# Kernel optimization log

Hardware: AMD Instinct MI355X
Metric: run time of the kernel (lower is better)

Reference implementation:

```python
import jax, jax.numpy as jnp
import numpy as np


def setup_inputs() -> dict:
    key = jax.random.key(0)
    k1, k2 = jax.random.split(key)
    f = jax.random.normal(k1, (4, 8192, 3), dtype=jnp.float32)
    f_ = jax.random.normal(k2, (4, 8192, 3), dtype=jnp.float32)
    return {"f": f, "f_": f_}


def _square_distance(src, dst):
    # src: [B,N,3], dst: [B,M,3] -> [B,N,M]
    # ||s-d||^2 = ||s||^2 + ||d||^2 - 2 s.d
    cross = jnp.einsum("bnc,bmc->bnm", src, dst)  # [B,N,M]
    s2 = jnp.sum(src * src, axis=-1)[:, :, None]   # [B,N,1]
    d2 = jnp.sum(dst * dst, axis=-1)[:, None, :]   # [B,1,M]
    return s2 + d2 - 2.0 * cross


def reference(f, f_):
    dis = _square_distance(f, f_)
    dis = jnp.maximum(dis, 0.0)  # dis[dis <= 0] = 0
    f2f_ = jnp.min(dis, axis=2)  # [B,N] nearest in f_ for each point of f
    f_2f = jnp.min(dis, axis=1)  # [B,M] nearest in f for each point of f_
    d = jnp.mean(f2f_, axis=1) + jnp.mean(f_2f, axis=1)  # [B]
    return jnp.mean(d)
```

## Files before the change

kernel.cpp:

```cpp
#include <hip/hip_runtime.h>

#define NPTS  8192
#define BATCH 4

typedef short  bf8    __attribute__((ext_vector_type(8)));
typedef float  f32x16 __attribute__((ext_vector_type(16)));
typedef float  v2f    __attribute__((ext_vector_type(2)));

__device__ inline unsigned short bf16_rne(float x) {
    unsigned u = __float_as_uint(x);
    unsigned r = (u + 0x7FFFu + ((u >> 16) & 1u)) >> 16;
    return (unsigned short)r;
}
__device__ inline float bf16_to_f(unsigned short h) {
    return __uint_as_float(((unsigned)h) << 16);
}
__device__ inline unsigned fenc(float x) {
    unsigned b = __float_as_uint(x);
    return (b & 0x80000000u) ? ~b : (b | 0x80000000u);
}
__device__ inline float fdec(unsigned k) {
    unsigned b = (k & 0x80000000u) ? (k ^ 0x80000000u) : ~k;
    return __uint_as_float(b);
}
template <int CTRL>
__device__ inline float dpp_mov(float x) {
    int i = __float_as_int(x);
    int r = __builtin_amdgcn_update_dpp(i, i, CTRL, 0xF, 0xF, false);
    return __int_as_float(r);
}
__device__ inline float redmax16(f32x16 v) {
    float a = fmaxf(v[0], v[1]),  b = fmaxf(v[2], v[3]);
    float c = fmaxf(v[4], v[5]),  d = fmaxf(v[6], v[7]);
    float e = fmaxf(v[8], v[9]),  f = fmaxf(v[10], v[11]);
    float g = fmaxf(v[12], v[13]), h = fmaxf(v[14], v[15]);
    float ab = fmaxf(a, b), cd = fmaxf(c, d);
    float ef = fmaxf(e, f), gh = fmaxf(g, h);
    return fmaxf(fmaxf(ab, cd), fmaxf(ef, gh));
}


__global__ void pack_mfma(const float* __restrict__ f, const float* __restrict__ f_,
                          bf8* __restrict__ fA, bf8* __restrict__ gB,
                          unsigned* __restrict__ seg, float* __restrict__ out) {
    int j = blockIdx.x * blockDim.x + threadIdx.x;
    if (j == 0) out[0] = 0.0f;
    seg[j] = 0u;
    int cloud = j >> 15;
    int idx   = j & 32767;
    const float* src = cloud ? f_ : f;
    float x = src[idx * 3 + 0], y = src[idx * 3 + 1], z = src[idx * 3 + 2];
    float w = -0.5f * (x * x + y * y + z * z);
    unsigned short xh = bf16_rne(x), yh = bf16_rne(y), zh = bf16_rne(z);
    unsigned short xl = bf16_rne(x - bf16_to_f(xh));
    unsigned short yl = bf16_rne(y - bf16_to_f(yh));
    unsigned short zl = bf16_rne(z - bf16_to_f(zh));
    unsigned short wh = bf16_rne(w);
    unsigned short wl = bf16_rne(w - bf16_to_f(wh));
    const short ONE = (short)0x3F80;

    int b = idx >> 13, p = idx & 8191;
    int t = p >> 5, li = p & 31;
    size_t base = ((size_t)(b * 256 + t)) * 64;
    if (cloud == 0) {
        bf8 A0, A1;
        A0[0]=(short)xh; A0[1]=(short)yh; A0[2]=(short)zh; A0[3]=(short)xl;
        A0[4]=(short)yl; A0[5]=(short)zl; A0[6]=(short)xh; A0[7]=(short)yh;
        A1[0]=(short)zh; A1[1]=ONE;       A1[2]=ONE;       A1[3]=(short)wh;
        A1[4]=(short)wl; A1[5]=0;         A1[6]=0;         A1[7]=0;
        fA[base + li]      = A0;
        fA[base + 32 + li] = A1;
    } else {
        bf8 B0, B1;
        B0[0]=(short)xh; B0[1]=(short)yh; B0[2]=(short)zh; B0[3]=(short)xh;
        B0[4]=(short)yh; B0[5]=(short)zh; B0[6]=(short)xl; B0[7]=(short)yl;
        B1[0]=(short)zl; B1[1]=(short)wh; B1[2]=(short)wl; B1[3]=ONE;
        B1[4]=ONE;       B1[5]=0;         B1[6]=0;         B1[7]=0;
        gB[base + li]      = B0;
        gB[base + 32 + li] = B1;
    }
}

__global__ __launch_bounds__(512, 4) void chamfer_mfma(
        const bf8* __restrict__ fA, const bf8* __restrict__ gB,
        unsigned* __restrict__ seg) {
    __shared__ bf8 lbs[2048];
    __shared__ unsigned colacc[1024];

    int tid  = threadIdx.x;
    int wv   = tid >> 6, lane = tid & 63;
    int bx   = blockIdx.x;
    int mseg = bx & 7;
    int nblk = (bx >> 3) & 15;
    int b    = bx >> 7;

    bf8 a[2];
    f32x16 rmax[2];
    int nt_loc = nblk * 16 + wv * 2;
#pragma unroll
    for (int s = 0; s < 2; ++s) {
        a[s] = fA[(size_t)(b * 256 + nt_loc + s) * 64 + lane];
        rmax[s] = (f32x16)(-3.0e38f);
    }

    const bf8* __restrict__ bp = gB + ((size_t)(b * 256 + mseg * 32)) * 64;
#pragma unroll
    for (int k = 0; k < 4; ++k) lbs[k * 512 + tid] = bp[k * 512 + tid];
    colacc[tid]       = 0u;
    colacc[tid + 512] = 0u;
    __syncthreads();

    f32x16 zc = (f32x16)(0.0f);
    unsigned* cp = &colacc[lane & 31];
    bf8 qa = lbs[lane];
    bf8 qb = lbs[64 + lane];
#pragma unroll 2
    for (int i = 0; i < 16; ++i) {
        int ip = (i + 1) & 15;
        bf8 na = lbs[ip * 128 + lane];
        bf8 nb = lbs[ip * 128 + 64 + lane];
        f32x16 d00 = __builtin_amdgcn_mfma_f32_32x32x16_bf16(a[0], qa, zc, 0, 0, 0);
        f32x16 d01 = __builtin_amdgcn_mfma_f32_32x32x16_bf16(a[0], qb, zc, 0, 0, 0);
        rmax[0] = __builtin_elementwise_max(
                      __builtin_elementwise_max(rmax[0], d00), d01);
        float t00 = redmax16(d00);
        float t01 = redmax16(d01);
        __builtin_amdgcn_sched_barrier(0);
        f32x16 d10 = __builtin_amdgcn_mfma_f32_32x32x16_bf16(a[1], qa, zc, 0, 0, 0);
        f32x16 d11 = __builtin_amdgcn_mfma_f32_32x32x16_bf16(a[1], qb, zc, 0, 0, 0);
        rmax[1] = __builtin_elementwise_max(
                      __builtin_elementwise_max(rmax[1], d10), d11);
        atomicMax(cp + i * 64,      fenc(fmaxf(t00, redmax16(d10))));
        atomicMax(cp + i * 64 + 32, fenc(fmaxf(t01, redmax16(d11))));
        __builtin_amdgcn_sched_barrier(0);
        qa = na; qb = nb;
    }

#pragma unroll
    for (int s = 0; s < 2; ++s) {
#pragma unroll
        for (int r = 0; r < 16; ++r) {
            float x = rmax[s][r];
            x = fmaxf(x, dpp_mov<0xB1>(x));
            x = fmaxf(x, dpp_mov<0x4E>(x));
            x = fmaxf(x, dpp_mov<0x124>(x));
            x = fmaxf(x, dpp_mov<0x128>(x));
            x = fmaxf(x, dpp_mov<0x142>(x));
            rmax[s][r] = x;
        }
    }

    if ((lane & 31) == 16) {
        int rbase = (lane >> 5) * 4;
        unsigned* sg = seg + (size_t)b * NPTS;
#pragma unroll
        for (int s = 0; s < 2; ++s) {
            int n0 = (nt_loc + s) * 32;
#pragma unroll
            for (int r = 0; r < 16; ++r) {
                int row = (r & 3) + 8 * (r >> 2) + rbase;
                atomicMax(&sg[n0 + row], fenc(rmax[s][r]));
            }
        }
    }

    __syncthreads();
    {
        unsigned* sg = seg + (size_t)(4 + b) * NPTS + mseg * 1024;
        atomicMax(&sg[tid],       colacc[tid]);
        atomicMax(&sg[tid + 512], colacc[tid + 512]);
    }
}

__global__ __launch_bounds__(1024) void finalize_mfma(
        const unsigned* __restrict__ seg, float* __restrict__ out) {
    __shared__ float partial[16];
    int j = blockIdx.x * 1024 + threadIdx.x;
    float emax = fdec(seg[j]);
    float dist = fmaxf(-2.0f * emax, 0.0f);
    for (int off = 32; off > 0; off >>= 1)
        dist += __shfl_down(dist, off, 64);
    int lane = threadIdx.x & 63, wv = threadIdx.x >> 6;
    if (lane == 0) partial[wv] = dist;
    __syncthreads();
    if (threadIdx.x < 16) {
        float s = partial[threadIdx.x];
        for (int off = 8; off > 0; off >>= 1)
            s += __shfl_down(s, off, 64);
        if (threadIdx.x == 0) atomicAdd(out, s * (1.0f / 32768.0f));
    }
}


__global__ void pack_pk(const float* __restrict__ f, const float* __restrict__ f_,
                        float4* __restrict__ pk, float* __restrict__ prf,
                        float* __restrict__ out) {
    int j = blockIdx.x * blockDim.x + threadIdx.x;
    if (j == 0) out[0] = 0.0f;
    const float* src = (j >= 32768) ? f_ : f;
    int idx = j & 32767;
    float x = src[idx * 3 + 0], y = src[idx * 3 + 1], z = src[idx * 3 + 2];
    float w = -0.5f * (x * x + y * y + z * z);
    pk[j] = make_float4(x, y, z, w);
    int  slot = j & 1;
    long base = (long)(j >> 1) * 8;
    prf[base + 0 + slot] = x;
    prf[base + 2 + slot] = y;
    prf[base + 4 + slot] = z;
    prf[base + 6 + slot] = w;
}

__global__ __launch_bounds__(512, 8) void chamfer_pk(
        const float4* __restrict__ pk, const float4* __restrict__ pr,
        float* __restrict__ seg) {
    __shared__ float red[8][256];
    int tid  = threadIdx.x;
    int wv   = __builtin_amdgcn_readfirstlane(tid >> 6);
    int lane = tid & 63;
    int bx   = blockIdx.x;
    int tile = bx & 31;
    int b    = (bx >> 5) & 3;
    int dir  = (bx >> 7) & 1;
    int mq   = bx >> 8;

    const float4* __restrict__ A = pk + ((size_t)dir * BATCH + b) * NPTS;
    int n_base = tile * 256;
    v2f px[4], py[4], pz[4], e2[4];
#pragma unroll
    for (int r = 0; r < 4; ++r) {
        float4 p = A[n_base + lane + 64 * r];
        px[r] = (v2f){p.x, p.x};
        py[r] = (v2f){p.y, p.y};
        pz[r] = (v2f){p.z, p.z};
        e2[r] = (v2f){-1e30f, -1e30f};
    }
    int sb_m = (1 - dir) * BATCH + b;
    const float4* __restrict__ mp =
        pr + ((size_t)sb_m * 4096 + mq * 1024 + wv * 128) * 2;

    for (int i = 0; i < 128; i += 4) {
#pragma unroll
        for (int u = 0; u < 4; ++u) {
            float4 qa = mp[(i + u) * 2 + 0];
            float4 qb = mp[(i + u) * 2 + 1];
            v2f qx = (v2f){qa.x, qa.y};
            v2f qy = (v2f){qa.z, qa.w};
            v2f qz = (v2f){qb.x, qb.y};
            v2f qw = (v2f){qb.z, qb.w};
#pragma unroll
            for (int r = 0; r < 4; ++r) {
                v2f c = __builtin_elementwise_fma(px[r], qx, qw);
                c = __builtin_elementwise_fma(py[r], qy, c);
                c = __builtin_elementwise_fma(pz[r], qz, c);
                e2[r] = __builtin_elementwise_max(e2[r], c);
            }
        }
    }
#pragma unroll
    for (int r = 0; r < 4; ++r)
        red[wv][lane + 64 * r] = fmaxf(e2[r].x, e2[r].y);
    __syncthreads();
    if (tid < 256) {
        float emax = red[0][tid];
#pragma unroll
        for (int ww = 1; ww < 8; ++ww) emax = fmaxf(emax, red[ww][tid]);
        seg[mq * (2 * BATCH * NPTS) + dir * (BATCH * NPTS) + b * NPTS
            + n_base + tid] = emax;
    }
}

__global__ __launch_bounds__(1024) void finalize_pk(
        const float4* __restrict__ pk, const float* __restrict__ seg,
        float* __restrict__ out) {
    __shared__ float partial[16];
    int j = blockIdx.x * 1024 + threadIdx.x;
    float emax = seg[j];
#pragma unroll
    for (int q = 1; q < 4; ++q) emax = fmaxf(emax, seg[q * 65536 + j]);
    float dist = fmaxf(-2.0f * (emax + pk[j].w), 0.0f);
    for (int off = 32; off > 0; off >>= 1)
        dist += __shfl_down(dist, off, 64);
    int lane = threadIdx.x & 63, wv = threadIdx.x >> 6;
    if (lane == 0) partial[wv] = dist;
    __syncthreads();
    if (threadIdx.x < 16) {
        float s = partial[threadIdx.x];
        for (int off = 8; off > 0; off >>= 1)
            s += __shfl_down(s, off, 64);
        if (threadIdx.x == 0) atomicAdd(out, s * (1.0f / 32768.0f));
    }
}


__global__ void zero_out_kernel(float* __restrict__ out) { out[0] = 0.0f; }

__global__ __launch_bounds__(1024) void chamfer_fallback(
        const float* __restrict__ f, const float* __restrict__ f_,
        float* __restrict__ out) {
    __shared__ float wlds[NPTS];
    __shared__ float red[16][256];
    __shared__ float partial[4];
    int tid  = threadIdx.x;
    int wv   = __builtin_amdgcn_readfirstlane(tid >> 6);
    int lane = tid & 63;
    int bx   = blockIdx.x;
    int dir  = bx >> 7;
    int b    = (bx >> 5) & 3;
    int tile = bx & 31;
    int n_base = tile * 256;
    const float* __restrict__ A  = dir ? f_ : f;
    const float* __restrict__ Bm = dir ? f  : f_;
    const float* an = A  + (size_t)b * NPTS * 3;
    const float* bm = Bm + (size_t)b * NPTS * 3;
    for (int i = tid; i < NPTS; i += 1024) {
        float x = bm[i * 3 + 0], y = bm[i * 3 + 1], z = bm[i * 3 + 2];
        wlds[i] = -0.5f * (x * x + y * y + z * z);
    }
    float xn[4], yn[4], zn[4];
#pragma unroll
    for (int r = 0; r < 4; ++r) {
        int n = n_base + lane + 64 * r;
        xn[r] = an[n * 3 + 0]; yn[r] = an[n * 3 + 1]; zn[r] = an[n * 3 + 2];
    }
    __syncthreads();
    float e[4];
#pragma unroll
    for (int r = 0; r < 4; ++r) e[r] = -1e30f;
    int m0 = wv * (NPTS / 16);
#pragma unroll 4
    for (int i = 0; i < NPTS / 16; ++i) {
        int m = m0 + i;
        float qx = bm[m * 3 + 0], qy = bm[m * 3 + 1], qz = bm[m * 3 + 2];
        float qw = wlds[m];
#pragma unroll
        for (int r = 0; r < 4; ++r) {
            float c = fmaf(zn[r], qz, fmaf(yn[r], qy, fmaf(xn[r], qx, qw)));
            e[r] = fmaxf(e[r], c);
        }
    }
#pragma unroll
    for (int r = 0; r < 4; ++r) red[wv][lane + 64 * r] = e[r];
    __syncthreads();
    if (tid < 256) {
        float emax = red[0][tid];
#pragma unroll
        for (int ww = 1; ww < 16; ++ww) emax = fmaxf(emax, red[ww][tid]);
        int n = n_base + tid;
        float x = an[n * 3 + 0], y = an[n * 3 + 1], z = an[n * 3 + 2];
        float dist = fmaxf(x * x + y * y + z * z - 2.0f * emax, 0.0f);
        for (int off = 32; off > 0; off >>= 1)
            dist += __shfl_down(dist, off, 64);
        if ((tid & 63) == 0) partial[tid >> 6] = dist;
    }
    __syncthreads();
    if (tid == 0) {
        float s = partial[0] + partial[1] + partial[2] + partial[3];
        atomicAdd(out, s * (1.0f / 32768.0f));
    }
}

extern "C" void kernel_launch(void* const* d_in, const int* in_sizes, int n_in,
                              void* d_out, int out_size, void* d_ws, size_t ws_size,
                              hipStream_t stream) {
    const float* f  = (const float*)d_in[0];
    const float* f_ = (const float*)d_in[1];
    float* out = (float*)d_out;

    const size_t MB = 1048576;
    if (ws_size >= 5 * MB) {
        bf8*      fA  = (bf8*)d_ws;
        bf8*      gB  = (bf8*)((char*)d_ws + 1 * MB);
        unsigned* seg = (unsigned*)((char*)d_ws + 2 * MB);
        pack_mfma<<<256, 256, 0, stream>>>(f, f_, fA, gB, seg, out);
        chamfer_mfma<<<512, 512, 0, stream>>>(fA, gB, seg);
        finalize_mfma<<<64, 1024, 0, stream>>>(seg, out);
    } else if (ws_size >= 3 * MB) {
        float4* pk = (float4*)d_ws;
        float4* pr = (float4*)((char*)d_ws + 1 * MB);
        float*  sg = (float*)((char*)d_ws + 2 * MB);
        pack_pk<<<256, 256, 0, stream>>>(f, f_, pk, (float*)pr, out);
        chamfer_pk<<<1024, 512, 0, stream>>>(pk, pr, sg);
        finalize_pk<<<64, 1024, 0, stream>>>(pk, sg, out);
    } else {
        zero_out_kernel<<<1, 1, 0, stream>>>(out);
        chamfer_fallback<<<256, 1024, 0, stream>>>(f, f_, out);
    }
}
```

Baseline: 84.15 us.

## Fuse bf16 packing into chamfer kernel and replace global atomics with partial buffers

```diff
diff --git a/kernel.cpp b/kernel.cpp
--- a/kernel.cpp
+++ b/kernel.cpp
@@ -40,52 +40,12 @@
 }
 
 
-__global__ void pack_mfma(const float* __restrict__ f, const float* __restrict__ f_,
-                          bf8* __restrict__ fA, bf8* __restrict__ gB,
-                          unsigned* __restrict__ seg, float* __restrict__ out) {
-    int j = blockIdx.x * blockDim.x + threadIdx.x;
-    if (j == 0) out[0] = 0.0f;
-    seg[j] = 0u;
-    int cloud = j >> 15;
-    int idx   = j & 32767;
-    const float* src = cloud ? f_ : f;
-    float x = src[idx * 3 + 0], y = src[idx * 3 + 1], z = src[idx * 3 + 2];
-    float w = -0.5f * (x * x + y * y + z * z);
-    unsigned short xh = bf16_rne(x), yh = bf16_rne(y), zh = bf16_rne(z);
-    unsigned short xl = bf16_rne(x - bf16_to_f(xh));
-    unsigned short yl = bf16_rne(y - bf16_to_f(yh));
-    unsigned short zl = bf16_rne(z - bf16_to_f(zh));
-    unsigned short wh = bf16_rne(w);
-    unsigned short wl = bf16_rne(w - bf16_to_f(wh));
-    const short ONE = (short)0x3F80;
-
-    int b = idx >> 13, p = idx & 8191;
-    int t = p >> 5, li = p & 31;
-    size_t base = ((size_t)(b * 256 + t)) * 64;
-    if (cloud == 0) {
-        bf8 A0, A1;
-        A0[0]=(short)xh; A0[1]=(short)yh; A0[2]=(short)zh; A0[3]=(short)xl;
-        A0[4]=(short)yl; A0[5]=(short)zl; A0[6]=(short)xh; A0[7]=(short)yh;
-        A1[0]=(short)zh; A1[1]=ONE;       A1[2]=ONE;       A1[3]=(short)wh;
-        A1[4]=(short)wl; A1[5]=0;         A1[6]=0;         A1[7]=0;
-        fA[base + li]      = A0;
-        fA[base + 32 + li] = A1;
-    } else {
-        bf8 B0, B1;
-        B0[0]=(short)xh; B0[1]=(short)yh; B0[2]=(short)zh; B0[3]=(short)xh;
-        B0[4]=(short)yh; B0[5]=(short)zh; B0[6]=(short)xl; B0[7]=(short)yl;
-        B1[0]=(short)zl; B1[1]=(short)wh; B1[2]=(short)wl; B1[3]=ONE;
-        B1[4]=ONE;       B1[5]=0;         B1[6]=0;         B1[7]=0;
-        gB[base + li]      = B0;
-        gB[base + 32 + li] = B1;
-    }
-}
-
-__global__ __launch_bounds__(512, 4) void chamfer_mfma(
-        const bf8* __restrict__ fA, const bf8* __restrict__ gB,
-        unsigned* __restrict__ seg) {
+__global__ __launch_bounds__(512, 4) void chamfer_fused(
+        const float* __restrict__ f, const float* __restrict__ f_,
+        float* __restrict__ fpart, float* __restrict__ gpart,
+        float* __restrict__ out) {
     __shared__ bf8 lbs[2048];
-    __shared__ unsigned colacc[1024];
+    __shared__ unsigned colacc2[2048];
 
     int tid  = threadIdx.x;
     int wv   = tid >> 6, lane = tid & 63;
@@ -94,24 +54,70 @@
     int nblk = (bx >> 3) & 15;
     int b    = bx >> 7;
 
+    if (bx == 0 && tid == 0) out[0] = 0.0f;
+
+    const short ONE = (short)0x3F80;
+
     bf8 a[2];
     f32x16 rmax[2];
     int nt_loc = nblk * 16 + wv * 2;
+    const float* __restrict__ fa = f + (size_t)b * NPTS * 3;
 #pragma unroll
     for (int s = 0; s < 2; ++s) {
-        a[s] = fA[(size_t)(b * 256 + nt_loc + s) * 64 + lane];
+        int p = (nt_loc + s) * 32 + (lane & 31);
+        const float* sp = fa + (size_t)p * 3;
+        float x = sp[0], y = sp[1], z = sp[2];
+        float w = -0.5f * (x * x + y * y + z * z);
+        unsigned short xh = bf16_rne(x), yh = bf16_rne(y), zh = bf16_rne(z);
+        unsigned short xl = bf16_rne(x - bf16_to_f(xh));
+        unsigned short yl = bf16_rne(y - bf16_to_f(yh));
+        unsigned short zl = bf16_rne(z - bf16_to_f(zh));
+        unsigned short wh = bf16_rne(w);
+        unsigned short wl = bf16_rne(w - bf16_to_f(wh));
+        bf8 av;
+        if (lane < 32) {
+            av[0]=(short)xh; av[1]=(short)yh; av[2]=(short)zh; av[3]=(short)xl;
+            av[4]=(short)yl; av[5]=(short)zl; av[6]=(short)xh; av[7]=(short)yh;
+        } else {
+            av[0]=(short)zh; av[1]=ONE;       av[2]=ONE;       av[3]=(short)wh;
+            av[4]=(short)wl; av[5]=0;         av[6]=0;         av[7]=0;
+        }
+        a[s] = av;
         rmax[s] = (f32x16)(-3.0e38f);
     }
 
-    const bf8* __restrict__ bp = gB + ((size_t)(b * 256 + mseg * 32)) * 64;
-#pragma unroll
-    for (int k = 0; k < 4; ++k) lbs[k * 512 + tid] = bp[k * 512 + tid];
-    colacc[tid]       = 0u;
-    colacc[tid + 512] = 0u;
+    const float* __restrict__ fb =
+        f_ + (size_t)b * NPTS * 3 + (size_t)mseg * 1024 * 3;
+#pragma unroll
+    for (int h = 0; h < 2; ++h) {
+        int p = tid + h * 512;
+        const float* sp = fb + (size_t)p * 3;
+        float x = sp[0], y = sp[1], z = sp[2];
+        float w = -0.5f * (x * x + y * y + z * z);
+        unsigned short xh = bf16_rne(x), yh = bf16_rne(y), zh = bf16_rne(z);
+        unsigned short xl = bf16_rne(x - bf16_to_f(xh));
+        unsigned short yl = bf16_rne(y - bf16_to_f(yh));
+        unsigned short zl = bf16_rne(z - bf16_to_f(zh));
+        unsigned short wh = bf16_rne(w);
+        unsigned short wl = bf16_rne(w - bf16_to_f(wh));
+        bf8 B0, B1;
+        B0[0]=(short)xh; B0[1]=(short)yh; B0[2]=(short)zh; B0[3]=(short)xh;
+        B0[4]=(short)yh; B0[5]=(short)zh; B0[6]=(short)xl; B0[7]=(short)yl;
+        B1[0]=(short)zl; B1[1]=(short)wh; B1[2]=(short)wl; B1[3]=ONE;
+        B1[4]=ONE;       B1[5]=0;         B1[6]=0;         B1[7]=0;
+        int t = p >> 5, li = p & 31;
+        lbs[t * 64 + li]      = B0;
+        lbs[t * 64 + 32 + li] = B1;
+    }
+    colacc2[tid]        = 0u;
+    colacc2[tid + 512]  = 0u;
+    colacc2[tid + 1024] = 0u;
+    colacc2[tid + 1536] = 0u;
     __syncthreads();
 
     f32x16 zc = (f32x16)(0.0f);
-    unsigned* cp = &colacc[lane & 31];
+    int half = lane >> 5, col = lane & 31;
+    unsigned* cp = &colacc2[half * 1024 + col];
     bf8 qa = lbs[lane];
     bf8 qb = lbs[64 + lane];
 #pragma unroll 2
@@ -123,15 +129,15 @@
         f32x16 d01 = __builtin_amdgcn_mfma_f32_32x32x16_bf16(a[0], qb, zc, 0, 0, 0);
         rmax[0] = __builtin_elementwise_max(
                       __builtin_elementwise_max(rmax[0], d00), d01);
-        float t00 = redmax16(d00);
-        float t01 = redmax16(d01);
+        float r0a = redmax16(d00);
+        float r1a = redmax16(d01);
         __builtin_amdgcn_sched_barrier(0);
         f32x16 d10 = __builtin_amdgcn_mfma_f32_32x32x16_bf16(a[1], qa, zc, 0, 0, 0);
         f32x16 d11 = __builtin_amdgcn_mfma_f32_32x32x16_bf16(a[1], qb, zc, 0, 0, 0);
         rmax[1] = __builtin_elementwise_max(
                       __builtin_elementwise_max(rmax[1], d10), d11);
-        atomicMax(cp + i * 64,      fenc(fmaxf(t00, redmax16(d10))));
-        atomicMax(cp + i * 64 + 32, fenc(fmaxf(t01, redmax16(d11))));
+        atomicMax(cp + i * 64,      fenc(fmaxf(r0a, redmax16(d10))));
+        atomicMax(cp + i * 64 + 32, fenc(fmaxf(r1a, redmax16(d11))));
         __builtin_amdgcn_sched_barrier(0);
         qa = na; qb = nb;
     }
@@ -149,34 +155,50 @@
             rmax[s][r] = x;
         }
     }
-
     if ((lane & 31) == 16) {
         int rbase = (lane >> 5) * 4;
-        unsigned* sg = seg + (size_t)b * NPTS;
+        float* fp = fpart + (size_t)mseg * (BATCH * NPTS) + (size_t)b * NPTS;
 #pragma unroll
         for (int s = 0; s < 2; ++s) {
             int n0 = (nt_loc + s) * 32;
 #pragma unroll
             for (int r = 0; r < 16; ++r) {
                 int row = (r & 3) + 8 * (r >> 2) + rbase;
-                atomicMax(&sg[n0 + row], fenc(rmax[s][r]));
+                fp[n0 + row] = rmax[s][r];
             }
         }
     }
 
     __syncthreads();
     {
-        unsigned* sg = seg + (size_t)(4 + b) * NPTS + mseg * 1024;
-        atomicMax(&sg[tid],       colacc[tid]);
-        atomicMax(&sg[tid + 512], colacc[tid + 512]);
-    }
-}
-
-__global__ __launch_bounds__(1024) void finalize_mfma(
-        const unsigned* __restrict__ seg, float* __restrict__ out) {
+        float* gp = gpart + (size_t)nblk * (BATCH * NPTS) + (size_t)b * NPTS
+                    + (size_t)mseg * 1024;
+#pragma unroll
+        for (int h = 0; h < 2; ++h) {
+            int j = tid + h * 512;
+            gp[j] = fmaxf(fdec(colacc2[j]), fdec(colacc2[1024 + j]));
+        }
+    }
+}
+
+__global__ __launch_bounds__(1024) void finalize_fused(
+        const float* __restrict__ fpart, const float* __restrict__ gpart,
+        float* __restrict__ out) {
     __shared__ float partial[16];
     int j = blockIdx.x * 1024 + threadIdx.x;
-    float emax = fdec(seg[j]);
+    float emax;
+    if (j < 32768) {
+        emax = fpart[j];
+#pragma unroll
+        for (int s = 1; s < 8; ++s)
+            emax = fmaxf(emax, fpart[s * 32768 + j]);
+    } else {
+        int jj = j - 32768;
+        emax = gpart[jj];
+#pragma unroll
+        for (int t = 1; t < 16; ++t)
+            emax = fmaxf(emax, gpart[t * 32768 + jj]);
+    }
     float dist = fmaxf(-2.0f * emax, 0.0f);
     for (int off = 32; off > 0; off >>= 1)
         dist += __shfl_down(dist, off, 64);
@@ -368,12 +390,10 @@
 
     const size_t MB = 1048576;
     if (ws_size >= 5 * MB) {
-        bf8*      fA  = (bf8*)d_ws;
-        bf8*      gB  = (bf8*)((char*)d_ws + 1 * MB);
-        unsigned* seg = (unsigned*)((char*)d_ws + 2 * MB);
-        pack_mfma<<<256, 256, 0, stream>>>(f, f_, fA, gB, seg, out);
-        chamfer_mfma<<<512, 512, 0, stream>>>(fA, gB, seg);
-        finalize_mfma<<<64, 1024, 0, stream>>>(seg, out);
+        float* fpart = (float*)d_ws;
+        float* gpart = (float*)((char*)d_ws + 1 * MB);
+        chamfer_fused<<<512, 512, 0, stream>>>(f, f_, fpart, gpart, out);
+        finalize_fused<<<64, 1024, 0, stream>>>(fpart, gpart, out);
     } else if (ws_size >= 3 * MB) {
         float4* pk = (float4*)d_ws;
         float4* pr = (float4*)((char*)d_ws + 1 * MB);
```

New measurement: 79.37 us, median of 2. 1.06x faster.
